# Performance work log

Measured on AMD Instinct MI355X. Metric: run time of the kernel, lower is better.

## Reference

```python
import jax, jax.numpy as jnp
import numpy as np

N_HEADS = 16


def apply_rotary_emb(x, cos, sin):
    # x: [B, H, S, hd]; cos/sin: [S, hd//2] (broadcast over B, H)
    xr = x.reshape(x.shape[:-1] + (-1, 2))
    r, i = xr[..., 0], xr[..., 1]
    a = r * cos - i * sin
    b = i * cos + r * sin
    return jnp.stack([a, b], axis=-1).reshape(x.shape).astype(x.dtype)


def setup_inputs() -> dict:
    key = jax.random.key(0)
    ks = jax.random.split(key, 7)
    B, S, D = 2, 2048, 1024
    hd = D // N_HEADS
    x = jax.random.normal(ks[0], (B, S, D), dtype=jnp.float32)
    freqs_cos = jax.random.uniform(ks[1], (S, hd // 2), dtype=jnp.float32)
    freqs_sin = jax.random.uniform(ks[2], (S, hd // 2), dtype=jnp.float32)
    sc = 1.0 / np.sqrt(D)
    Wq = jax.random.normal(ks[3], (D, D), dtype=jnp.float32) * sc
    Wk = jax.random.normal(ks[4], (D, D), dtype=jnp.float32) * sc
    Wv = jax.random.normal(ks[5], (D, D), dtype=jnp.float32) * sc
    Wo = jax.random.normal(ks[6], (D, D), dtype=jnp.float32) * sc
    return {"x": x, "freqs_cos": freqs_cos, "freqs_sin": freqs_sin,
            "Wq": Wq, "Wk": Wk, "Wv": Wv, "Wo": Wo}


def reference(x, freqs_cos, freqs_sin, Wq, Wk, Wv, Wo):
    B, S, D = x.shape
    H = N_HEADS
    hd = D // H
    # QKV projections (nn.Linear: x @ W.T)
    q = (x @ Wq.T).reshape(B, S, H, hd).transpose(0, 2, 1, 3)
    k = (x @ Wk.T).reshape(B, S, H, hd).transpose(0, 2, 1, 3)
    v = (x @ Wv.T).reshape(B, S, H, hd).transpose(0, 2, 1, 3)
    q = apply_rotary_emb(q, freqs_cos, freqs_sin)
    k = apply_rotary_emb(k, freqs_cos, freqs_sin)
    # causal SDPA (scale = 1/sqrt(head_dim), as in F.scaled_dot_product_attention)
    scores = jnp.einsum("bhqd,bhkd->bhqk", q, k) * (1.0 / np.sqrt(hd))
    causal = jnp.tril(jnp.ones((S, S), dtype=bool))
    scores = jnp.where(causal, scores, -jnp.inf)
    probs = jax.nn.softmax(scores, axis=-1)
    attn_out = jnp.einsum("bhqk,bhkd->bhqd", probs, v)
    attn_cat = attn_out.transpose(0, 2, 1, 3).reshape(B, S, D)
    return attn_cat @ Wo.T
```

## Files before the change

### kernel.cpp

```cpp
#include <hip/hip_runtime.h>
#include <hip/hip_bf16.h>
#include <cstdint>

typedef __attribute__((ext_vector_type(8))) short short8;
typedef __attribute__((ext_vector_type(4))) float f32x4;

#define B_  2
#define S_  2048
#define D_  1024
#define H_  16
#define HD  64

static __device__ __forceinline__ float bf2f(unsigned int u16) {
    union { unsigned int i; float f; } v; v.i = u16 << 16; return v.f;
}
static __device__ __forceinline__ unsigned short f2bf(float f) {
    union { float f; unsigned int i; } v; v.f = f;
    unsigned int r = v.i + 0x7FFFu + ((v.i >> 16) & 1u);
    return (unsigned short)(r >> 16);
}
static __device__ __forceinline__ unsigned pack_bf16(float hi, float lo) {
    union { float f; unsigned u; } h, l;
    h.f = hi; l.f = lo;
    return __builtin_amdgcn_perm(h.u + 0x8000u, l.u + 0x8000u, 0x07060302);
}
static __device__ __forceinline__ void load_lds_16B(const unsigned short* g, unsigned short* l) {
    __builtin_amdgcn_global_load_lds(
        (const __attribute__((address_space(1))) unsigned int*)g,
        (__attribute__((address_space(3))) unsigned int*)l, 16, 0, 0);
}

__global__ void cvt_f32_bf16(const float* __restrict__ src,
                             unsigned short* __restrict__ dst, int n4) {
    int i = blockIdx.x * 256 + threadIdx.x;
    if (i >= n4) return;
    float4 f = ((const float4*)src)[i];
    uint2 o;
    o.x = (unsigned int)f2bf(f.x) | ((unsigned int)f2bf(f.y) << 16);
    o.y = (unsigned int)f2bf(f.z) | ((unsigned int)f2bf(f.w) << 16);
    ((uint2*)dst)[i] = o;
}

__global__ void cvt_w4(const float* __restrict__ w0, const float* __restrict__ w1,
                       const float* __restrict__ w2, const float* __restrict__ w3,
                       unsigned short* __restrict__ dst) {
    int bid = blockIdx.x;
    int wsel = bid >> 10;
    const float* s = wsel == 0 ? w0 : wsel == 1 ? w1 : wsel == 2 ? w2 : w3;
    int i = (bid & 1023) * 256 + threadIdx.x;
    float4 f = ((const float4*)s)[i];
    uint2 o;
    o.x = (unsigned int)f2bf(f.x) | ((unsigned int)f2bf(f.y) << 16);
    o.y = (unsigned int)f2bf(f.z) | ((unsigned int)f2bf(f.w) << 16);
    ((uint2*)dst)[(size_t)wsel * 262144 + i] = o;
}

__global__ __launch_bounds__(256) void qkv_gemm(
    const unsigned short* __restrict__ xbf,
    const unsigned short* __restrict__ wq,
    const unsigned short* __restrict__ wk,
    const unsigned short* __restrict__ wv,
    unsigned short* __restrict__ qb,
    unsigned short* __restrict__ kb,
    unsigned short* __restrict__ vb)
{
    __shared__ unsigned short As[128 * 32];
    __shared__ unsigned short Bs[128 * 32];

    const int tid  = threadIdx.x;
    const int w    = tid >> 6, lane = tid & 63;
    const int l15  = lane & 15, quad = lane >> 4;
    const int wrow = (w >> 1) * 64, wcol = (w & 1) * 64;

    const int m0 = blockIdx.x * 128;
    const int nc = blockIdx.y * 128;
    const int sel = nc >> 10;
    const int n0 = nc & 1023;
    const unsigned short* __restrict__ W = sel == 0 ? wq : (sel == 1 ? wk : wv);
    unsigned short* __restrict__ Out = sel == 0 ? qb : (sel == 1 ? kb : vb);

    const int lr = lane >> 2, lc = (lane & 3) * 8;
    const unsigned short* ga = xbf + (size_t)(m0 + w * 16 + lr) * 1024 + lc;
    const unsigned short* gb = W   + (size_t)(n0 + w * 16 + lr) * 1024 + lc;
    unsigned short* la0 = As + (w * 16) * 32;
    unsigned short* la1 = As + (64 + w * 16) * 32;
    unsigned short* lb0 = Bs + (w * 16) * 32;
    unsigned short* lb1 = Bs + (64 + w * 16) * 32;

    f32x4 acc[4][4] = {};

    for (int k0 = 0; k0 < 1024; k0 += 32) {
        __syncthreads();
        load_lds_16B(ga + k0,             la0);
        load_lds_16B(ga + 64 * 1024 + k0, la1);
        load_lds_16B(gb + k0,             lb0);
        load_lds_16B(gb + 64 * 1024 + k0, lb1);
        __syncthreads();

        short8 a[4], b[4];
#pragma unroll
        for (int i = 0; i < 4; i++)
            a[i] = *(const short8*)&As[(wrow + i * 16 + l15) * 32 + quad * 8];
#pragma unroll
        for (int j = 0; j < 4; j++)
            b[j] = *(const short8*)&Bs[(wcol + j * 16 + l15) * 32 + quad * 8];
#pragma unroll
        for (int i = 0; i < 4; i++)
#pragma unroll
            for (int j = 0; j < 4; j++)
                acc[i][j] = __builtin_amdgcn_mfma_f32_16x16x32_bf16(a[i], b[j], acc[i][j], 0, 0, 0);
    }

#pragma unroll
    for (int i = 0; i < 4; i++) {
#pragma unroll
        for (int r = 0; r < 4; r++) {
            int m = m0 + wrow + i * 16 + quad * 4 + r;
            int bb = m >> 11, s = m & 2047;
#pragma unroll
            for (int j = 0; j < 4; j++) {
                int n = n0 + wcol + j * 16 + l15;
                int h = n >> 6, d = n & 63;
                Out[(((size_t)(bb * H_ + h) * S_) + s) * HD + d] = f2bf(acc[i][j][r]);
            }
        }
    }
}

__global__ __launch_bounds__(256) void out_gemm(
    const unsigned short* __restrict__ A,
    const unsigned short* __restrict__ Bt,
    float* __restrict__ C)
{
    __shared__ unsigned short As[128 * 32];
    __shared__ unsigned short Bs[128 * 32];

    const int tid  = threadIdx.x;
    const int w    = tid >> 6, lane = tid & 63;
    const int l15  = lane & 15, quad = lane >> 4;
    const int wrow = (w >> 1) * 64, wcol = (w & 1) * 64;

    const int m0 = blockIdx.x * 128;
    const int n0 = blockIdx.y * 128;

    const int lr = lane >> 2, lc = (lane & 3) * 8;
    const unsigned short* ga = A  + (size_t)(m0 + w * 16 + lr) * 1024 + lc;
    const unsigned short* gb = Bt + (size_t)(n0 + w * 16 + lr) * 1024 + lc;
    unsigned short* la0 = As + (w * 16) * 32;
    unsigned short* la1 = As + (64 + w * 16) * 32;
    unsigned short* lb0 = Bs + (w * 16) * 32;
    unsigned short* lb1 = Bs + (64 + w * 16) * 32;

    f32x4 acc[4][4] = {};

    for (int k0 = 0; k0 < 1024; k0 += 32) {
        __syncthreads();
        load_lds_16B(ga + k0,             la0);
        load_lds_16B(ga + 64 * 1024 + k0, la1);
        load_lds_16B(gb + k0,             lb0);
        load_lds_16B(gb + 64 * 1024 + k0, lb1);
        __syncthreads();

        short8 a[4], b[4];
#pragma unroll
        for (int i = 0; i < 4; i++)
            a[i] = *(const short8*)&As[(wrow + i * 16 + l15) * 32 + quad * 8];
#pragma unroll
        for (int j = 0; j < 4; j++)
            b[j] = *(const short8*)&Bs[(wcol + j * 16 + l15) * 32 + quad * 8];
#pragma unroll
        for (int i = 0; i < 4; i++)
#pragma unroll
            for (int j = 0; j < 4; j++)
                acc[i][j] = __builtin_amdgcn_mfma_f32_16x16x32_bf16(a[i], b[j], acc[i][j], 0, 0, 0);
    }

#pragma unroll
    for (int i = 0; i < 4; i++)
#pragma unroll
        for (int r = 0; r < 4; r++) {
            int m = m0 + wrow + i * 16 + quad * 4 + r;
#pragma unroll
            for (int j = 0; j < 4; j++)
                C[(size_t)m * 1024 + n0 + wcol + j * 16 + l15] = acc[i][j][r];
        }
}

__global__ void rope_qk(unsigned short* __restrict__ qb,
                        unsigned short* __restrict__ kb,
                        const float* __restrict__ fcos,
                        const float* __restrict__ fsin)
{
    int idx = blockIdx.x * 256 + threadIdx.x;
    int t  = idx & 31;
    int s  = (idx >> 5) & (S_ - 1);
    int bh = idx >> 16;
    float c  = fcos[s * 32 + t];
    float si = fsin[s * 32 + t];
    size_t off = ((size_t)bh * S_ + s) * HD + 2 * t;

    unsigned int* qp = (unsigned int*)(qb + off);
    unsigned int u = *qp;
    float r = bf2f(u & 0xffffu), im = bf2f(u >> 16);
    *qp = pack_bf16(im * c + r * si, r * c - im * si);

    unsigned int* kp = (unsigned int*)(kb + off);
    u = *kp;
    r = bf2f(u & 0xffffu); im = bf2f(u >> 16);
    *kp = pack_bf16(im * c + r * si, r * c - im * si);
}

__global__ __launch_bounds__(256) void flash_attn_mfma(
    const unsigned short* __restrict__ qb,
    const unsigned short* __restrict__ kb,
    const unsigned short* __restrict__ vb,
    unsigned short* __restrict__ attnc)
{
    __shared__ unsigned short Ks[2][64][32];
    __shared__ unsigned short Vt[64][72];
    __shared__ unsigned short Pls[4][16][72];

    const int bh   = blockIdx.x;
    const int qt   = blockIdx.y;
    const int b    = bh >> 4, h = bh & 15;
    const int tid  = threadIdx.x;
    const int w    = tid >> 6;
    const int lane = tid & 63;
    const int l15  = lane & 15;
    const int quad = lane >> 4;

    const size_t bhS = (size_t)bh * S_;

    short8 qfrag[2];
    {
        const unsigned short* qp = qb + (bhS + qt * 64 + w * 16 + l15) * HD + quad * 8;
        qfrag[0] = *(const short8*)(qp);
        qfrag[1] = *(const short8*)(qp + 32);
    }

    const int klr = lane >> 2, klc = (lane & 3) * 8;
    const int vdg = tid >> 5, vp = tid & 31;

    f32x4 O[4] = {};
    float mrow = -INFINITY;
    float lrow = 0.0f;
    const float sc = 0.125f * 1.44269504f;

    for (int jt = 0; jt <= qt; jt++) {
        const int j0 = jt * 64;
        {
            const unsigned short* kg = kb + (bhS + j0 + w * 16 + klr) * HD + klc;
            load_lds_16B(kg,      &Ks[0][w * 16][0]);
            load_lds_16B(kg + 32, &Ks[1][w * 16][0]);
        }
        {
            const unsigned short* vptr = vb + (bhS + j0 + 2 * vp) * HD + vdg * 8;
            uint4 v0 = *(const uint4*)vptr;
            uint4 v1 = *(const uint4*)(vptr + HD);
            const unsigned* a0 = (const unsigned*)&v0;
            const unsigned* a1 = (const unsigned*)&v1;
#pragma unroll
            for (int c = 0; c < 4; c++) {
                *(unsigned*)&Vt[vdg * 8 + 2 * c][2 * vp] =
                    __builtin_amdgcn_perm(a1[c], a0[c], 0x05040100);
                *(unsigned*)&Vt[vdg * 8 + 2 * c + 1][2 * vp] =
                    __builtin_amdgcn_perm(a1[c], a0[c], 0x07060302);
            }
        }
        __syncthreads();

        const bool diag  = (jt == qt);
        const int  nsub  = diag ? (w + 1) : 4;
        const int  kgmax = (nsub + 1) >> 1;

        f32x4 Sacc[4];
        float tmax = -INFINITY;
        for (int sub = 0; sub < nsub; sub++) {
            f32x4 s = {};
#pragma unroll
            for (int kh = 0; kh < 2; kh++) {
                short8 kf = *(const short8*)&Ks[kh][sub * 16 + l15][quad * 8];
                s = __builtin_amdgcn_mfma_f32_16x16x32_bf16(kf, qfrag[kh], s, 0, 0, 0);
            }
#pragma unroll
            for (int r = 0; r < 4; r++) {
                float v = s[r] * sc;
                if (diag && (sub * 16 + quad * 4 + r > w * 16 + l15)) v = -INFINITY;
                s[r] = v;
                tmax = fmaxf(tmax, v);
            }
            Sacc[sub] = s;
        }
        tmax = fmaxf(tmax, __shfl_xor(tmax, 16, 64));
        tmax = fmaxf(tmax, __shfl_xor(tmax, 32, 64));

        float mnew = fmaxf(mrow, tmax);
        float ccr  = __builtin_amdgcn_exp2f(mrow - mnew);

        float psum = 0.0f;
        for (int sub = 0; sub < nsub; sub++) {
            f32x4 s = Sacc[sub];
            float p0 = __builtin_amdgcn_exp2f(s[0] - mnew);
            float p1 = __builtin_amdgcn_exp2f(s[1] - mnew);
            float p2 = __builtin_amdgcn_exp2f(s[2] - mnew);
            float p3 = __builtin_amdgcn_exp2f(s[3] - mnew);
            psum += (p0 + p1) + (p2 + p3);
            uint2 pk;
            pk.x = pack_bf16(p1, p0);
            pk.y = pack_bf16(p3, p2);
            *(uint2*)&Pls[w][l15][sub * 16 + quad * 4] = pk;
        }
        if (diag) {
            for (int sub = nsub; sub < 2 * kgmax; sub++) {
                uint2 z; z.x = 0u; z.y = 0u;
                *(uint2*)&Pls[w][l15][sub * 16 + quad * 4] = z;
            }
        }
        psum += __shfl_xor(psum, 16, 64);
        psum += __shfl_xor(psum, 32, 64);
        lrow = lrow * ccr + psum;
        mrow = mnew;

#pragma unroll
        for (int r = 0; r < 4; r++) {
            float ccq = __shfl(ccr, quad * 4 + r, 64);
#pragma unroll
            for (int dt = 0; dt < 4; dt++) O[dt][r] *= ccq;
        }

        for (int kg = 0; kg < kgmax; kg++) {
            short8 pf = *(const short8*)&Pls[w][l15][kg * 32 + quad * 8];
#pragma unroll
            for (int dt = 0; dt < 4; dt++) {
                short8 vf = *(const short8*)&Vt[dt * 16 + l15][kg * 32 + quad * 8];
                O[dt] = __builtin_amdgcn_mfma_f32_16x16x32_bf16(pf, vf, O[dt], 0, 0, 0);
            }
        }
        __syncthreads();
    }

    float inv = 1.0f / lrow;
#pragma unroll
    for (int r = 0; r < 4; r++) {
        float invq = __shfl(inv, quad * 4 + r, 64);
        int qabs = qt * 64 + w * 16 + quad * 4 + r;
        unsigned short* op = attnc + (((size_t)b * S_ + qabs) * H_ + h) * HD + l15;
#pragma unroll
        for (int dt = 0; dt < 4; dt++)
            op[dt * 16] = f2bf(O[dt][r] * invq);
    }
}

extern "C" void kernel_launch(void* const* d_in, const int* in_sizes, int n_in,
                              void* d_out, int out_size, void* d_ws, size_t ws_size,
                              hipStream_t stream) {
    const float* x    = (const float*)d_in[0];
    const float* fcos = (const float*)d_in[1];
    const float* fsin = (const float*)d_in[2];
    const float* Wq   = (const float*)d_in[3];
    const float* Wk   = (const float*)d_in[4];
    const float* Wv   = (const float*)d_in[5];
    const float* Wo   = (const float*)d_in[6];
    float* out = (float*)d_out;

    unsigned short* ws = (unsigned short*)d_ws;
    unsigned short* xbf = ws;
    unsigned short* wqb = xbf + 4096 * 1024;
    unsigned short* wkb = wqb + 1024 * 1024;
    unsigned short* wvb = wkb + 1024 * 1024;
    unsigned short* wob = wvb + 1024 * 1024;
    unsigned short* qb  = wob + 1024 * 1024;
    unsigned short* kb  = qb + 4096 * 1024;
    unsigned short* vb  = kb + 4096 * 1024;
    unsigned short* attnc = vb + 4096 * 1024;

    cvt_f32_bf16<<<4096, 256, 0, stream>>>(x, xbf, 4096 * 1024 / 4);
    cvt_w4<<<4096, 256, 0, stream>>>(Wq, Wk, Wv, Wo, wqb);

    qkv_gemm<<<dim3(32, 24), 256, 0, stream>>>(xbf, wqb, wkb, wvb, qb, kb, vb);

    rope_qk<<<8192, 256, 0, stream>>>(qb, kb, fcos, fsin);

    flash_attn_mfma<<<dim3(32, 32), 256, 0, stream>>>(qb, kb, vb, attnc);

    out_gemm<<<dim3(32, 8), 256, 0, stream>>>(attnc, wob, out);
}
```

Before: 230.2 us.

## Pre-transpose V, swizzle LDS tiles, balance causal tiles, lazily rescale softmax

Adds a separate kernel that writes V transposed into the free x-bf16 workspace. The attention kernel can then load V tiles directly into LDS with async 16-byte loads, with no in-loop register transpose. K and V LDS tiles use XOR swizzles to avoid bank conflicts, and query-tile indices are remapped so heavy and light causal tiles interleave. The online-softmax rescale of O and l now runs only when the running max grows by more than a threshold, saving shuffles and multiplies but letting exponent inputs drift above zero. The extra launch and the write and read of transposed V add memory traffic.

```diff
diff --git a/kernel.cpp b/kernel.cpp
--- a/kernel.cpp
+++ b/kernel.cpp
@@ -210,18 +210,49 @@
     *kp = pack_bf16(im * c + r * si, r * c - im * si);
 }
 
+__global__ __launch_bounds__(256) void v_transpose(
+    const unsigned short* __restrict__ vb,
+    unsigned short* __restrict__ vT)
+{
+    __shared__ unsigned short T[64][72];
+    const int bh = blockIdx.x;
+    const int j0 = blockIdx.y * 64;
+    const int tid = threadIdx.x;
+    const int vdg = tid >> 5, vp = tid & 31;
+    const unsigned short* vptr = vb + ((size_t)bh * S_ + j0 + 2 * vp) * HD + vdg * 8;
+    uint4 v0 = *(const uint4*)vptr;
+    uint4 v1 = *(const uint4*)(vptr + HD);
+    const unsigned* a0 = (const unsigned*)&v0;
+    const unsigned* a1 = (const unsigned*)&v1;
+#pragma unroll
+    for (int c = 0; c < 4; c++) {
+        *(unsigned*)&T[vdg * 8 + 2 * c][2 * vp]     = __builtin_amdgcn_perm(a1[c], a0[c], 0x05040100);
+        *(unsigned*)&T[vdg * 8 + 2 * c + 1][2 * vp] = __builtin_amdgcn_perm(a1[c], a0[c], 0x07060302);
+    }
+    __syncthreads();
+    const int d = tid >> 3, js = (tid & 7) * 8;
+#pragma unroll
+    for (int dd = 0; dd < 2; dd++) {
+        short8 row = *(const short8*)&T[dd * 32 + d][js];
+        *(short8*)(vT + ((size_t)bh * HD + dd * 32 + d) * S_ + j0 + js) = row;
+    }
+}
+
 __global__ __launch_bounds__(256) void flash_attn_mfma(
     const unsigned short* __restrict__ qb,
     const unsigned short* __restrict__ kb,
-    const unsigned short* __restrict__ vb,
+    const unsigned short* __restrict__ vT,
     unsigned short* __restrict__ attnc)
 {
-    __shared__ unsigned short Ks[2][64][32];
-    __shared__ unsigned short Vt[64][72];
+    __shared__ __attribute__((aligned(1024))) unsigned short Ks[2][64][32];
+    __shared__ __attribute__((aligned(1024))) unsigned short Vt[64][64];
     __shared__ unsigned short Pls[4][16][72];
 
     const int bh   = blockIdx.x;
-    const int qt   = blockIdx.y;
+    const int qtb  = blockIdx.y;
+    const int jj = qtb & 7, mm = qtb >> 3;
+    const int qt = (mm == 0) ? jj : (mm == 1) ? 31 - jj : (mm == 2) ? 8 + jj : 23 - jj;
+
     const int b    = bh >> 4, h = bh & 15;
     const int tid  = threadIdx.x;
     const int w    = tid >> 6;
@@ -230,6 +261,7 @@
     const int quad = lane >> 4;
 
     const size_t bhS = (size_t)bh * S_;
+    const unsigned short* __restrict__ vTb = vT + (size_t)bh * HD * S_;
 
     short8 qfrag[2];
     {
@@ -238,8 +270,13 @@
         qfrag[1] = *(const short8*)(qp + 32);
     }
 
-    const int klr = lane >> 2, klc = (lane & 3) * 8;
-    const int vdg = tid >> 5, vp = tid & 31;
+    const int ksrow  = lane >> 2;
+    const int ksslot = (lane & 3) ^ ((lane >> 3) & 3);
+    const int vsrow  = lane >> 3;
+    const int vsslot = (lane & 7) ^ vsrow;
+
+    const int ckq = (quad ^ ((l15 >> 1) & 3)) << 4;
+    const int s7  = l15 & 7;
 
     f32x4 O[4] = {};
     float mrow = -INFINITY;
@@ -249,23 +286,14 @@
     for (int jt = 0; jt <= qt; jt++) {
         const int j0 = jt * 64;
         {
-            const unsigned short* kg = kb + (bhS + j0 + w * 16 + klr) * HD + klc;
+            const unsigned short* kg = kb + (bhS + j0 + w * 16 + ksrow) * HD + ksslot * 8;
             load_lds_16B(kg,      &Ks[0][w * 16][0]);
             load_lds_16B(kg + 32, &Ks[1][w * 16][0]);
         }
         {
-            const unsigned short* vptr = vb + (bhS + j0 + 2 * vp) * HD + vdg * 8;
-            uint4 v0 = *(const uint4*)vptr;
-            uint4 v1 = *(const uint4*)(vptr + HD);
-            const unsigned* a0 = (const unsigned*)&v0;
-            const unsigned* a1 = (const unsigned*)&v1;
-#pragma unroll
-            for (int c = 0; c < 4; c++) {
-                *(unsigned*)&Vt[vdg * 8 + 2 * c][2 * vp] =
-                    __builtin_amdgcn_perm(a1[c], a0[c], 0x05040100);
-                *(unsigned*)&Vt[vdg * 8 + 2 * c + 1][2 * vp] =
-                    __builtin_amdgcn_perm(a1[c], a0[c], 0x07060302);
-            }
+            const unsigned short* vg = vTb + (size_t)(w * 16 + vsrow) * S_ + j0 + vsslot * 8;
+            load_lds_16B(vg,          &Vt[w * 16][0]);
+            load_lds_16B(vg + 8 * S_, &Vt[w * 16 + 8][0]);
         }
         __syncthreads();
 
@@ -279,7 +307,8 @@
             f32x4 s = {};
 #pragma unroll
             for (int kh = 0; kh < 2; kh++) {
-                short8 kf = *(const short8*)&Ks[kh][sub * 16 + l15][quad * 8];
+                int bo = ((sub * 16 + l15) << 6) + ckq;
+                short8 kf = *(const short8*)((const char*)&Ks[kh][0][0] + bo);
                 s = __builtin_amdgcn_mfma_f32_16x16x32_bf16(kf, qfrag[kh], s, 0, 0, 0);
             }
 #pragma unroll
@@ -294,16 +323,26 @@
         tmax = fmaxf(tmax, __shfl_xor(tmax, 16, 64));
         tmax = fmaxf(tmax, __shfl_xor(tmax, 32, 64));
 
-        float mnew = fmaxf(mrow, tmax);
-        float ccr  = __builtin_amdgcn_exp2f(mrow - mnew);
+        if (__any(tmax > mrow + 8.0f)) {
+            float mnew = fmaxf(mrow, tmax);
+            float ccr  = __builtin_amdgcn_exp2f(mrow - mnew);
+            lrow *= ccr;
+#pragma unroll
+            for (int r = 0; r < 4; r++) {
+                float ccq = __shfl(ccr, quad * 4 + r, 64);
+#pragma unroll
+                for (int dt = 0; dt < 4; dt++) O[dt][r] *= ccq;
+            }
+            mrow = mnew;
+        }
 
         float psum = 0.0f;
         for (int sub = 0; sub < nsub; sub++) {
             f32x4 s = Sacc[sub];
-            float p0 = __builtin_amdgcn_exp2f(s[0] - mnew);
-            float p1 = __builtin_amdgcn_exp2f(s[1] - mnew);
-            float p2 = __builtin_amdgcn_exp2f(s[2] - mnew);
-            float p3 = __builtin_amdgcn_exp2f(s[3] - mnew);
+            float p0 = __builtin_amdgcn_exp2f(s[0] - mrow);
+            float p1 = __builtin_amdgcn_exp2f(s[1] - mrow);
+            float p2 = __builtin_amdgcn_exp2f(s[2] - mrow);
+            float p3 = __builtin_amdgcn_exp2f(s[3] - mrow);
             psum += (p0 + p1) + (p2 + p3);
             uint2 pk;
             pk.x = pack_bf16(p1, p0);
@@ -318,21 +357,15 @@
         }
         psum += __shfl_xor(psum, 16, 64);
         psum += __shfl_xor(psum, 32, 64);
-        lrow = lrow * ccr + psum;
-        mrow = mnew;
-
-#pragma unroll
-        for (int r = 0; r < 4; r++) {
-            float ccq = __shfl(ccr, quad * 4 + r, 64);
-#pragma unroll
-            for (int dt = 0; dt < 4; dt++) O[dt][r] *= ccq;
-        }
+        lrow += psum;
 
         for (int kg = 0; kg < kgmax; kg++) {
             short8 pf = *(const short8*)&Pls[w][l15][kg * 32 + quad * 8];
 #pragma unroll
             for (int dt = 0; dt < 4; dt++) {
-                short8 vf = *(const short8*)&Vt[dt * 16 + l15][kg * 32 + quad * 8];
+                int row = dt * 16 + l15;
+                int slot = (((kg << 2) | quad) ^ s7) << 4;
+                short8 vf = *(const short8*)((const char*)&Vt[0][0] + (row << 7) + slot);
                 O[dt] = __builtin_amdgcn_mfma_f32_16x16x32_bf16(pf, vf, O[dt], 0, 0, 0);
             }
         }
@@ -373,15 +406,18 @@
     unsigned short* kb  = qb + 4096 * 1024;
     unsigned short* vb  = kb + 4096 * 1024;
     unsigned short* attnc = vb + 4096 * 1024;
+    unsigned short* vT = xbf;
 
     cvt_f32_bf16<<<4096, 256, 0, stream>>>(x, xbf, 4096 * 1024 / 4);
     cvt_w4<<<4096, 256, 0, stream>>>(Wq, Wk, Wv, Wo, wqb);
 
     qkv_gemm<<<dim3(32, 24), 256, 0, stream>>>(xbf, wqb, wkb, wvb, qb, kb, vb);
 
+    v_transpose<<<dim3(32, 32), 256, 0, stream>>>(vb, vT);
+
     rope_qk<<<8192, 256, 0, stream>>>(qb, kb, fcos, fsin);
 
-    flash_attn_mfma<<<dim3(32, 32), 256, 0, stream>>>(qb, kb, vb, attnc);
+    flash_attn_mfma<<<dim3(32, 32), 256, 0, stream>>>(qb, kb, vT, attnc);
 
     out_gemm<<<dim3(32, 8), 256, 0, stream>>>(attnc, wob, out);
 }
```

New measurement: 215.9 us. -6.2%, faster.
